# Kernel tuning notes

Hardware: AMD Instinct MI355X
Metric: run time of the kernel (lower is better)

## Reference

```python
import jax, jax.numpy as jnp
import numpy as np

N = 50000
E = 800000
IN_DIM = 256
HID = 64
HEADS = 4
OUT = 64
NEG_SLOPE = 0.2


def _gat_layer(x, src, dst, W, a_src, a_dst, b, heads, out_ch, concat):
    n = x.shape[0]
    h = (x @ W).reshape(n, heads, out_ch)                      # [N,H,C]
    al_src = jnp.sum(h * a_src, axis=-1)                       # [N,H]
    al_dst = jnp.sum(h * a_dst, axis=-1)                       # [N,H]
    e = jax.nn.leaky_relu(al_src[src] + al_dst[dst], NEG_SLOPE)  # [E,H]
    # segment softmax over destination nodes
    m = jax.ops.segment_max(e, dst, num_segments=n)
    m = jnp.where(jnp.isfinite(m), m, 0.0)
    ex = jnp.exp(e - m[dst])
    denom = jax.ops.segment_sum(ex, dst, num_segments=n)
    alpha = ex / (denom[dst] + 1e-16)                          # [E,H]
    msg = h[src] * alpha[:, :, None]                           # [E,H,C]
    out = jax.ops.segment_sum(msg, dst, num_segments=n)        # [N,H,C]
    out = out.reshape(n, heads * out_ch) if concat else out.mean(axis=1)
    return out + b


def setup_inputs() -> dict:
    key = jax.random.key(0)
    ks = jax.random.split(key, 16)
    x = jax.random.normal(ks[0], (N, IN_DIM), dtype=jnp.float32)
    edge_index = jax.random.randint(ks[1], (2, E), 0, N, dtype=jnp.int64)

    def glorot(k, shape):
        fan = shape[0] + shape[-1]
        s = jnp.sqrt(6.0 / fan).astype(jnp.float32)
        return jax.random.uniform(k, shape, jnp.float32, -s, s)

    # layer 1: IN_DIM -> HID x HEADS (concat)
    W1 = glorot(ks[2], (IN_DIM, HEADS * HID))
    a_src1 = glorot(ks[3], (HEADS, HID))
    a_dst1 = glorot(ks[4], (HEADS, HID))
    b1 = jnp.zeros((HEADS * HID,), jnp.float32)
    # layer 2: HID*HEADS -> HID x HEADS (concat)
    W2 = glorot(ks[5], (HEADS * HID, HEADS * HID))
    a_src2 = glorot(ks[6], (HEADS, HID))
    a_dst2 = glorot(ks[7], (HEADS, HID))
    b2 = jnp.zeros((HEADS * HID,), jnp.float32)
    # layer 3: HID*HEADS -> OUT, 1 head, concat=False
    W3 = glorot(ks[8], (HEADS * HID, OUT))
    a_src3 = glorot(ks[9], (1, OUT))
    a_dst3 = glorot(ks[10], (1, OUT))
    b3 = jnp.zeros((OUT,), jnp.float32)

    return {"x": x, "edge_index": edge_index,
            "W1": W1, "a_src1": a_src1, "a_dst1": a_dst1, "b1": b1,
            "W2": W2, "a_src2": a_src2, "a_dst2": a_dst2, "b2": b2,
            "W3": W3, "a_src3": a_src3, "a_dst3": a_dst3, "b3": b3}


def reference(x, edge_index, W1, a_src1, a_dst1, b1, W2, a_src2, a_dst2, b2, W3, a_src3, a_dst3, b3):
    src, dst = edge_index[0], edge_index[1]
    h = _gat_layer(x, src, dst, W1, a_src1, a_dst1, b1, HEADS, HID, True)
    h = jax.nn.elu(h)
    h = _gat_layer(h, src, dst, W2, a_src2, a_dst2, b2, HEADS, HID, True)
    h = jax.nn.elu(h)
    h = _gat_layer(h, src, dst, W3, a_src3, a_dst3, b3, 1, OUT, False)
    h = jax.nn.elu(h)
    return h
```

## Files before the change

### kernel.cpp

```cpp
#include <hip/hip_runtime.h>
#include <hip/hip_bf16.h>
#include <math.h>

#define IN_DIM 256
#define HID 64
#define HEADS 4
#define HC (HEADS * HID)
#define OUTC 64
#define NEG_SLOPE 0.2f

typedef unsigned int uint;
typedef unsigned short ushortt;
typedef __attribute__((ext_vector_type(8))) short short8v;
typedef __attribute__((ext_vector_type(4))) float floatx4;

union U8 { uint u[4]; short8v v; };

__device__ __forceinline__ float lrelu(float x) {
    return x >= 0.f ? x : NEG_SLOPE * x;
}
__device__ __forceinline__ float elu1(float x) {
    return x > 0.f ? x : expm1f(x);
}
__device__ __forceinline__ ushortt f2bf(float f) {
    uint x = __float_as_uint(f);
    uint r = (x + 0x7fffu + ((x >> 16) & 1u)) >> 16;
    return (ushortt)r;
}
__device__ __forceinline__ float bf2f(ushortt u) {
    return __uint_as_float(((uint)u) << 16);
}

#define CVTPAIR(fx, fy, ho, qo)                                                 \
    asm("v_cvt_pk_bf16_f32 %0, %1, %2" : "=v"(ho) : "v"(fx), "v"(fy));          \
    {                                                                           \
        float _r0 = (fx) - __uint_as_float((ho) << 16);                         \
        float _r1 = (fy) - __uint_as_float((ho) & 0xffff0000u);                 \
        asm("v_cvt_pk_bf16_f32 %0, %1, %2" : "=v"(qo) : "v"(_r0), "v"(_r1));    \
    }

__device__ __forceinline__ void wsplit_body(const float* __restrict__ W,
                                            ushortt* __restrict__ Wt, int N,
                                            int b, int tid) {
    int idx = b * 256 + tid;
    int j = idx & 7;
    int col = (idx >> 3) % N;
    int kb = (idx >> 3) / N;
    float wv = W[(size_t)(kb * 8 + j) * N + col];
    ushortt hi = f2bf(wv);
    ushortt lo = f2bf(wv - bf2f(hi));
    size_t o = ((size_t)kb * N + col) * 16 + j;
    Wt[o] = hi;
    Wt[o + 8] = lo;
}

__global__ __launch_bounds__(256) void count_prep(
        const float* __restrict__ W1, const float* __restrict__ W2,
        const float* __restrict__ W3,
        ushortt* __restrict__ Wt1, ushortt* __restrict__ Wt2,
        ushortt* __restrict__ Wt3,
        const int* __restrict__ dst, int* __restrict__ counts, int E) {
    int b = blockIdx.x, tid = threadIdx.x;
    if (b < 256) { wsplit_body(W1, Wt1, 256, b, tid); return; }
    if (b < 512) { wsplit_body(W2, Wt2, 256, b - 256, tid); return; }
    if (b < 576) { wsplit_body(W3, Wt3, 64, b - 512, tid); return; }
    int e = (b - 576) * 256 + tid;
    if (e < E) atomicAdd(&counts[dst[e]], 1);
}

#define SCAN_B 1024
__global__ void scan_block(const int* __restrict__ counts, int* __restrict__ ptr,
                           int* __restrict__ bsums, int n) {
    __shared__ int sm[SCAN_B];
    int b = blockIdx.x, t = threadIdx.x;
    int i = b * SCAN_B + t;
    int v = (i < n) ? counts[i] : 0;
    sm[t] = v;
    __syncthreads();
    for (int off = 1; off < SCAN_B; off <<= 1) {
        int add = (t >= off) ? sm[t - off] : 0;
        __syncthreads();
        sm[t] += add;
        __syncthreads();
    }
    if (i < n) ptr[i + 1] = sm[t];
    if (t == SCAN_B - 1) bsums[b] = sm[t];
}

__global__ void scan_add(int* __restrict__ ptr, const int* __restrict__ bsums,
                         int* __restrict__ work, int n) {
    __shared__ int pre;
    int seg = blockIdx.x >> 2;
    if (threadIdx.x == 0) {
        int s = 0;
        for (int b = 0; b < seg; b++) s += bsums[b];
        pre = s;
    }
    __syncthreads();
    int i = blockIdx.x * 256 + threadIdx.x;
    if (i == 0) { ptr[0] = 0; work[0] = 0; }
    if (i < n) {
        int v = ptr[i + 1] + pre;
        ptr[i + 1] = v;
        if (i + 1 < n) work[i + 1] = v;
    }
}

__global__ void scatter_edges(const int* __restrict__ src, const int* __restrict__ dst,
                              int* __restrict__ work, int* __restrict__ ssrc, int E) {
    int e = blockIdx.x * blockDim.x + threadIdx.x;
    if (e < E) {
        int p = atomicAdd(&work[dst[e]], 1);
        ssrc[p] = src[e] * 64;
    }
}

template<bool F32A>
__global__ __launch_bounds__(256, 3) void gemm_mfma(
        const ushortt* __restrict__ Ai, const float* __restrict__ Af,
        const ushortt* __restrict__ Wt,
        ushortt* __restrict__ Chi, int M,
        const float* __restrict__ a_src, const float* __restrict__ a_dst,
        float* __restrict__ alS, float* __restrict__ alD) {
    constexpr int N = 256;
    int t = threadIdx.x;
    int wid = t >> 6, l = t & 63, l15 = l & 15, chunk = l >> 4;
    int wr = wid >> 1, wc = wid & 1;
    int row0 = blockIdx.x * 64;
    int colw = wc * 128;

    floatx4 acc[2][8];
    floatx4 zero = {0.f, 0.f, 0.f, 0.f};
#pragma unroll
    for (int mt = 0; mt < 2; mt++)
#pragma unroll
        for (int nt = 0; nt < 8; nt++) acc[mt][nt] = zero;

    size_t arow[2];
#pragma unroll
    for (int mt = 0; mt < 2; mt++) {
        int r = row0 + wr * 32 + mt * 16 + l15;
        int rc = r < M ? r : M - 1;
        arow[mt] = F32A ? (size_t)rc * 256 : (size_t)rc * 512;
    }

    for (int ks = 0; ks < 8; ks++) {
        int kb = ks * 4 + chunk;
        short8v ah[2], aq[2];
        if constexpr (F32A) {
#pragma unroll
            for (int mt = 0; mt < 2; mt++) {
                const float* ap = Af + arow[mt] + kb * 8;
                float4 a0 = ((const float4*)ap)[0];
                float4 a1 = ((const float4*)ap)[1];
                U8 h, q;
                CVTPAIR(a0.x, a0.y, h.u[0], q.u[0]);
                CVTPAIR(a0.z, a0.w, h.u[1], q.u[1]);
                CVTPAIR(a1.x, a1.y, h.u[2], q.u[2]);
                CVTPAIR(a1.z, a1.w, h.u[3], q.u[3]);
                ah[mt] = h.v; aq[mt] = q.v;
            }
        } else {
#pragma unroll
            for (int mt = 0; mt < 2; mt++) {
                const ushortt* ap = Ai + arow[mt] + kb * 16;
                ah[mt] = *(const short8v*)ap;
                aq[mt] = *(const short8v*)(ap + 8);
            }
        }
        const ushortt* bbase = Wt + ((size_t)kb * N + colw + l15) * 16;
#pragma unroll
        for (int half = 0; half < 2; half++) {
            short8v bh[4], bq[4];
#pragma unroll
            for (int nt = 0; nt < 4; nt++) {
                const ushortt* bp = bbase + (size_t)(half * 4 + nt) * 256;
                bh[nt] = *(const short8v*)bp;
                bq[nt] = *(const short8v*)(bp + 8);
            }
#pragma unroll
            for (int mt = 0; mt < 2; mt++)
#pragma unroll
                for (int nt = 0; nt < 4; nt++) {
                    int c = half * 4 + nt;
                    acc[mt][c] = __builtin_amdgcn_mfma_f32_16x16x32_bf16(aq[mt], bh[nt], acc[mt][c], 0, 0, 0);
                    acc[mt][c] = __builtin_amdgcn_mfma_f32_16x16x32_bf16(ah[mt], bq[nt], acc[mt][c], 0, 0, 0);
                    acc[mt][c] = __builtin_amdgcn_mfma_f32_16x16x32_bf16(ah[mt], bh[nt], acc[mt][c], 0, 0, 0);
                }
        }
    }

#pragma unroll
    for (int mt = 0; mt < 2; mt++)
#pragma unroll
        for (int j = 0; j < 4; j++) {
            int r = row0 + wr * 32 + mt * 16 + chunk * 4 + j;
            if (r < M) {
#pragma unroll
                for (int nt = 0; nt < 8; nt++)
                    Chi[(size_t)r * N + colw + nt * 16 + l15] = f2bf(acc[mt][nt][j]);
            }
        }

    {
        float aSv[8], aDv[8];
#pragma unroll
        for (int nt = 0; nt < 8; nt++) {
            aSv[nt] = a_src[colw + nt * 16 + l15];
            aDv[nt] = a_dst[colw + nt * 16 + l15];
        }
#pragma unroll
        for (int mt = 0; mt < 2; mt++)
#pragma unroll
            for (int j = 0; j < 4; j++) {
                float s0 = 0.f, d0 = 0.f, s1 = 0.f, d1 = 0.f;
#pragma unroll
                for (int nt = 0; nt < 4; nt++) {
                    s0 += acc[mt][nt][j] * aSv[nt];
                    d0 += acc[mt][nt][j] * aDv[nt];
                    s1 += acc[mt][nt + 4][j] * aSv[nt + 4];
                    d1 += acc[mt][nt + 4][j] * aDv[nt + 4];
                }
#pragma unroll
                for (int off = 1; off < 16; off <<= 1) {
                    s0 += __shfl_xor(s0, off);
                    d0 += __shfl_xor(d0, off);
                    s1 += __shfl_xor(s1, off);
                    d1 += __shfl_xor(d1, off);
                }
                int r = row0 + wr * 32 + mt * 16 + chunk * 4 + j;
                if (l15 == 0 && r < M) {
                    alS[(size_t)r * 4 + wc * 2 + 0] = s0;
                    alS[(size_t)r * 4 + wc * 2 + 1] = s1;
                    alD[(size_t)r * 4 + wc * 2 + 0] = d0;
                    alD[(size_t)r * 4 + wc * 2 + 1] = d1;
                }
            }
    }
}

__global__ __launch_bounds__(256) void gemm_n64(
        const ushortt* __restrict__ Ai, const ushortt* __restrict__ Wt,
        ushortt* __restrict__ Chi, int M,
        const float* __restrict__ a_src, const float* __restrict__ a_dst,
        float* __restrict__ alS, float* __restrict__ alD) {
    constexpr int N = 64;
    int t = threadIdx.x;
    int wid = t >> 6, l = t & 63, l15 = l & 15, chunk = l >> 4;
    int row0 = blockIdx.x * 64;
    int rw = row0 + wid * 16 + l15;
    size_t arow = (size_t)(rw < M ? rw : M - 1) * 512;

    floatx4 acc[4];
    floatx4 zero = {0.f, 0.f, 0.f, 0.f};
#pragma unroll
    for (int nt = 0; nt < 4; nt++) acc[nt] = zero;

    for (int ks = 0; ks < 8; ks++) {
        int kb = ks * 4 + chunk;
        short8v bh[4], bq[4];
#pragma unroll
        for (int nt = 0; nt < 4; nt++) {
            const ushortt* bp = Wt + ((size_t)kb * N + nt * 16 + l15) * 16;
            bh[nt] = *(const short8v*)bp;
            bq[nt] = *(const short8v*)(bp + 8);
        }
        const ushortt* ap = Ai + arow + kb * 16;
        short8v ah = *(const short8v*)ap;
        short8v aq = *(const short8v*)(ap + 8);
#pragma unroll
        for (int nt = 0; nt < 4; nt++) {
            acc[nt] = __builtin_amdgcn_mfma_f32_16x16x32_bf16(aq, bh[nt], acc[nt], 0, 0, 0);
            acc[nt] = __builtin_amdgcn_mfma_f32_16x16x32_bf16(ah, bq[nt], acc[nt], 0, 0, 0);
            acc[nt] = __builtin_amdgcn_mfma_f32_16x16x32_bf16(ah, bh[nt], acc[nt], 0, 0, 0);
        }
    }

    float aSv[4], aDv[4];
#pragma unroll
    for (int nt = 0; nt < 4; nt++) {
        aSv[nt] = a_src[nt * 16 + l15];
        aDv[nt] = a_dst[nt * 16 + l15];
    }
#pragma unroll
    for (int j = 0; j < 4; j++) {
        int r = row0 + wid * 16 + chunk * 4 + j;
        if (r < M) {
#pragma unroll
            for (int nt = 0; nt < 4; nt++)
                Chi[(size_t)r * N + nt * 16 + l15] = f2bf(acc[nt][j]);
        }
        float s = 0.f, d = 0.f;
#pragma unroll
        for (int nt = 0; nt < 4; nt++) {
            s += acc[nt][j] * aSv[nt];
            d += acc[nt][j] * aDv[nt];
        }
#pragma unroll
        for (int off = 1; off < 16; off <<= 1) {
            s += __shfl_xor(s, off);
            d += __shfl_xor(d, off);
        }
        if (l15 == 0 && r < M) {
            alS[r] = s;
            alD[r] = d;
        }
    }
}

__global__ __launch_bounds__(256) void gather4f(
        const float* __restrict__ alS, const float* __restrict__ alD,
        const ushortt* __restrict__ h,
        const int* __restrict__ ptr, const int* __restrict__ ssrc,
        const float* __restrict__ bias, ushortt* __restrict__ outAi, int n) {
    int w = threadIdx.x >> 6, lane = threadIdx.x & 63;
    int node = blockIdx.x * 4 + w;
    if (node >= n) return;
    int p0 = ptr[node], p1 = ptr[node + 1];
    int head = lane >> 4;
    float adh = alD[node * 4 + head];
    const ushort4* h4 = (const ushort4*)h;
    float4 acc0 = make_float4(0.f, 0.f, 0.f, 0.f);
    float4 acc1 = make_float4(0.f, 0.f, 0.f, 0.f);
    float sum = 0.f;

    int i = p0;
#pragma unroll 1
    for (; i + 8 <= p1; i += 8) {
        int o0 = ssrc[i+0], o1 = ssrc[i+1], o2 = ssrc[i+2], o3 = ssrc[i+3];
        int o4 = ssrc[i+4], o5 = ssrc[i+5], o6 = ssrc[i+6], o7 = ssrc[i+7];
        float w0 = __expf(lrelu(alS[(o0 >> 4) + head] + adh));
        float w1 = __expf(lrelu(alS[(o1 >> 4) + head] + adh));
        float w2 = __expf(lrelu(alS[(o2 >> 4) + head] + adh));
        float w3 = __expf(lrelu(alS[(o3 >> 4) + head] + adh));
        float w4 = __expf(lrelu(alS[(o4 >> 4) + head] + adh));
        float w5 = __expf(lrelu(alS[(o5 >> 4) + head] + adh));
        float w6 = __expf(lrelu(alS[(o6 >> 4) + head] + adh));
        float w7 = __expf(lrelu(alS[(o7 >> 4) + head] + adh));
        ushort4 u0 = h4[o0 + lane];
        ushort4 u1 = h4[o1 + lane];
        ushort4 u2 = h4[o2 + lane];
        ushort4 u3 = h4[o3 + lane];
        ushort4 u4 = h4[o4 + lane];
        ushort4 u5 = h4[o5 + lane];
        ushort4 u6 = h4[o6 + lane];
        ushort4 u7 = h4[o7 + lane];
        sum += w0 + w1 + w2 + w3 + w4 + w5 + w6 + w7;
        acc0.x += bf2f(u0.x)*w0; acc0.y += bf2f(u0.y)*w0; acc0.z += bf2f(u0.z)*w0; acc0.w += bf2f(u0.w)*w0;
        acc1.x += bf2f(u1.x)*w1; acc1.y += bf2f(u1.y)*w1; acc1.z += bf2f(u1.z)*w1; acc1.w += bf2f(u1.w)*w1;
        acc0.x += bf2f(u2.x)*w2; acc0.y += bf2f(u2.y)*w2; acc0.z += bf2f(u2.z)*w2; acc0.w += bf2f(u2.w)*w2;
        acc1.x += bf2f(u3.x)*w3; acc1.y += bf2f(u3.y)*w3; acc1.z += bf2f(u3.z)*w3; acc1.w += bf2f(u3.w)*w3;
        acc0.x += bf2f(u4.x)*w4; acc0.y += bf2f(u4.y)*w4; acc0.z += bf2f(u4.z)*w4; acc0.w += bf2f(u4.w)*w4;
        acc1.x += bf2f(u5.x)*w5; acc1.y += bf2f(u5.y)*w5; acc1.z += bf2f(u5.z)*w5; acc1.w += bf2f(u5.w)*w5;
        acc0.x += bf2f(u6.x)*w6; acc0.y += bf2f(u6.y)*w6; acc0.z += bf2f(u6.z)*w6; acc0.w += bf2f(u6.w)*w6;
        acc1.x += bf2f(u7.x)*w7; acc1.y += bf2f(u7.y)*w7; acc1.z += bf2f(u7.z)*w7; acc1.w += bf2f(u7.w)*w7;
    }
#pragma unroll 1
    for (; i < p1; ++i) {
        int o0 = ssrc[i];
        float w0 = __expf(lrelu(alS[(o0 >> 4) + head] + adh));
        ushort4 u0 = h4[o0 + lane];
        sum += w0;
        acc0.x += bf2f(u0.x)*w0; acc0.y += bf2f(u0.y)*w0; acc0.z += bf2f(u0.z)*w0; acc0.w += bf2f(u0.w)*w0;
    }
    float invh = 1.f / (sum + 1e-16f);
    acc0.x = (acc0.x + acc1.x) * invh;
    acc0.y = (acc0.y + acc1.y) * invh;
    acc0.z = (acc0.z + acc1.z) * invh;
    acc0.w = (acc0.w + acc1.w) * invh;

    float4 b = ((const float4*)bias)[lane];
    float4 o;
    o.x = elu1(acc0.x + b.x);
    o.y = elu1(acc0.y + b.y);
    o.z = elu1(acc0.z + b.z);
    o.w = elu1(acc0.w + b.w);
    ushort4 oh, oq;
    oh.x = f2bf(o.x); oq.x = f2bf(o.x - bf2f(oh.x));
    oh.y = f2bf(o.y); oq.y = f2bf(o.y - bf2f(oh.y));
    oh.z = f2bf(o.z); oq.z = f2bf(o.z - bf2f(oh.z));
    oh.w = f2bf(o.w); oq.w = f2bf(o.w - bf2f(oh.w));
    size_t base = (size_t)node * 512 + (lane >> 1) * 16 + (lane & 1) * 4;
    *(ushort4*)&outAi[base] = oh;
    *(ushort4*)&outAi[base + 8] = oq;
}

__global__ __launch_bounds__(256) void gather1f(
        const float* __restrict__ alS, const float* __restrict__ alD,
        const ushortt* __restrict__ h,
        const int* __restrict__ ptr, const int* __restrict__ ssrc,
        const float* __restrict__ bias, float* __restrict__ out, int n) {
    int w = threadIdx.x >> 6, lane = threadIdx.x & 63;
    int node = blockIdx.x * 4 + w;
    if (node >= n) return;
    int p0 = ptr[node], p1 = ptr[node + 1];
    float ad = alD[node];
    int eslot = lane >> 4, cg = lane & 15;
    const ushort4* h4 = (const ushort4*)h;
    float4 acc = make_float4(0.f, 0.f, 0.f, 0.f);
    float sum = 0.f;

#pragma unroll 1
    for (int i = p0 + eslot; i < p1; i += 4) {
        int o = ssrc[i];
        float wv = __expf(lrelu(alS[o >> 6] + ad));
        ushort4 u = h4[(o >> 2) + cg];
        sum += wv;
        acc.x += bf2f(u.x) * wv;
        acc.y += bf2f(u.y) * wv;
        acc.z += bf2f(u.z) * wv;
        acc.w += bf2f(u.w) * wv;
    }
#pragma unroll
    for (int off = 16; off < 64; off <<= 1) {
        acc.x += __shfl_xor(acc.x, off);
        acc.y += __shfl_xor(acc.y, off);
        acc.z += __shfl_xor(acc.z, off);
        acc.w += __shfl_xor(acc.w, off);
        sum   += __shfl_xor(sum, off);
    }
    if (eslot == 0) {
        float inv = 1.f / (sum + 1e-16f);
        float4 b = ((const float4*)bias)[cg];
        float4 o;
        o.x = elu1(acc.x * inv + b.x);
        o.y = elu1(acc.y * inv + b.y);
        o.z = elu1(acc.z * inv + b.z);
        o.w = elu1(acc.w * inv + b.w);
        ((float4*)out)[node * 16 + cg] = o;
    }
}

extern "C" void kernel_launch(void* const* d_in, const int* in_sizes, int n_in,
                              void* d_out, int out_size, void* d_ws, size_t ws_size,
                              hipStream_t stream) {
    const float* x      = (const float*)d_in[0];
    const int*   eidx   = (const int*)d_in[1];
    const float* W1     = (const float*)d_in[2];
    const float* a_src1 = (const float*)d_in[3];
    const float* a_dst1 = (const float*)d_in[4];
    const float* b1     = (const float*)d_in[5];
    const float* W2     = (const float*)d_in[6];
    const float* a_src2 = (const float*)d_in[7];
    const float* a_dst2 = (const float*)d_in[8];
    const float* b2     = (const float*)d_in[9];
    const float* W3     = (const float*)d_in[10];
    const float* a_src3 = (const float*)d_in[11];
    const float* a_dst3 = (const float*)d_in[12];
    const float* b3     = (const float*)d_in[13];

    const int n = in_sizes[0] / IN_DIM;
    const int E = in_sizes[1] / 2;
    const int* srcp = eidx;
    const int* dstp = eidx + E;

    size_t off = 0;
    auto alloc = [&](size_t bytes) {
        void* p = (char*)d_ws + off;
        off += (bytes + 255) & ~(size_t)255;
        return p;
    };
    int*     ptr    = (int*)alloc((size_t)(n + 1) * 4);
    int*     work   = (int*)alloc((size_t)n * 4);
    int*     bsums  = (int*)alloc(256 * 4);
    int*     ssrc   = (int*)alloc((size_t)E * 4);
    ushortt* Ai0    = (ushortt*)alloc((size_t)n * 512 * 2);
    ushortt* Ai1    = (ushortt*)alloc((size_t)n * 512 * 2);
    ushortt* hbf    = (ushortt*)alloc((size_t)n * HC * 2);
    float*   alS    = (float*)alloc((size_t)n * HEADS * 4);
    float*   alD    = (float*)alloc((size_t)n * HEADS * 4);
    ushortt* Wt1    = (ushortt*)alloc((size_t)256 * HC * 2 * 2);
    ushortt* Wt2    = (ushortt*)alloc((size_t)256 * HC * 2 * 2);
    ushortt* Wt3    = (ushortt*)alloc((size_t)256 * OUTC * 2 * 2);
    (void)ws_size;

    hipMemsetAsync(work, 0, (size_t)n * 4, stream);
    int cblocks = 576 + (E + 255) / 256;
    count_prep<<<cblocks, 256, 0, stream>>>(W1, W2, W3, Wt1, Wt2, Wt3,
                                            dstp, work, E);
    int nb = (n + SCAN_B - 1) / SCAN_B;
    scan_block<<<nb, SCAN_B, 0, stream>>>(work, ptr, bsums, n);
    scan_add<<<(n + 255) / 256, 256, 0, stream>>>(ptr, bsums, work, n);
    scatter_edges<<<(E + 255) / 256, 256, 0, stream>>>(srcp, dstp, work, ssrc, E);

    int gblocks = (n + 63) / 64;
    int node4 = (n + 3) / 4;

    gemm_mfma<true><<<gblocks, 256, 0, stream>>>(
        nullptr, x, Wt1, hbf, n, a_src1, a_dst1, alS, alD);
    gather4f<<<node4, 256, 0, stream>>>(alS, alD, hbf, ptr, ssrc, b1, Ai1, n);

    gemm_mfma<false><<<gblocks, 256, 0, stream>>>(
        Ai1, nullptr, Wt2, hbf, n, a_src2, a_dst2, alS, alD);
    gather4f<<<node4, 256, 0, stream>>>(alS, alD, hbf, ptr, ssrc, b2, Ai0, n);

    gemm_n64<<<gblocks, 256, 0, stream>>>(
        Ai0, Wt3, hbf, n, a_src3, a_dst3, alS, alD);
    gather1f<<<node4, 256, 0, stream>>>(alS, alD, hbf, ptr, ssrc, b3,
                                        (float*)d_out, n);
}
```

Baseline: 386.1 us.

## Fuse CSR block scan into first GEMM launch and dedupe attention weights in gather

The standalone block-scan kernel is removed and its work is done by extra trailing blocks of the first layer's GEMM launch, each scanning 1024 counts with 256 threads holding four values apiece. This saves a launch and lets the scan run alongside the GEMM. In gather4f, each lane now computes one edge's attention weight, and the eight weights are broadcast with shuffles instead of every lane doing eight redundant alS loads and exps. The gather block size also drops from 256 to 128 threads (two nodes per block), giving finer scheduling granularity at the cost of more blocks.

```diff
diff --git a/kernel.cpp b/kernel.cpp
--- a/kernel.cpp
+++ b/kernel.cpp
@@ -68,25 +68,6 @@
     if (e < E) atomicAdd(&counts[dst[e]], 1);
 }
 
-#define SCAN_B 1024
-__global__ void scan_block(const int* __restrict__ counts, int* __restrict__ ptr,
-                           int* __restrict__ bsums, int n) {
-    __shared__ int sm[SCAN_B];
-    int b = blockIdx.x, t = threadIdx.x;
-    int i = b * SCAN_B + t;
-    int v = (i < n) ? counts[i] : 0;
-    sm[t] = v;
-    __syncthreads();
-    for (int off = 1; off < SCAN_B; off <<= 1) {
-        int add = (t >= off) ? sm[t - off] : 0;
-        __syncthreads();
-        sm[t] += add;
-        __syncthreads();
-    }
-    if (i < n) ptr[i + 1] = sm[t];
-    if (t == SCAN_B - 1) bsums[b] = sm[t];
-}
-
 __global__ void scan_add(int* __restrict__ ptr, const int* __restrict__ bsums,
                          int* __restrict__ work, int n) {
     __shared__ int pre;
@@ -121,8 +102,40 @@
         const ushortt* __restrict__ Wt,
         ushortt* __restrict__ Chi, int M,
         const float* __restrict__ a_src, const float* __restrict__ a_dst,
-        float* __restrict__ alS, float* __restrict__ alD) {
+        float* __restrict__ alS, float* __restrict__ alD,
+        const int* __restrict__ counts, int* __restrict__ ptrOut,
+        int* __restrict__ bsums, int nScan, int gemmBlocks) {
     constexpr int N = 256;
+    if constexpr (F32A) {
+        if ((int)blockIdx.x >= gemmBlocks) {
+            __shared__ int sm[256];
+            int sb = blockIdx.x - gemmBlocks;
+            int t = threadIdx.x;
+            int i = sb * 1024 + t * 4;
+            int v0 = 0, v1 = 0, v2 = 0, v3 = 0;
+            if (i + 0 < nScan) v0 = counts[i + 0];
+            if (i + 1 < nScan) v1 = counts[i + 1];
+            if (i + 2 < nScan) v2 = counts[i + 2];
+            if (i + 3 < nScan) v3 = counts[i + 3];
+            int s1 = v0 + v1, s2 = s1 + v2, s3 = s2 + v3;
+            sm[t] = s3;
+            __syncthreads();
+            for (int off = 1; off < 256; off <<= 1) {
+                int add = (t >= off) ? sm[t - off] : 0;
+                __syncthreads();
+                sm[t] += add;
+                __syncthreads();
+            }
+            int pre = (t > 0) ? sm[t - 1] : 0;
+            if (i + 0 < nScan) ptrOut[i + 1] = pre + v0;
+            if (i + 1 < nScan) ptrOut[i + 2] = pre + s1;
+            if (i + 2 < nScan) ptrOut[i + 3] = pre + s2;
+            if (i + 3 < nScan) ptrOut[i + 4] = pre + s3;
+            if (t == 255) bsums[sb] = sm[255];
+            return;
+        }
+    }
+
     int t = threadIdx.x;
     int wid = t >> 6, l = t & 63, l15 = l & 15, chunk = l >> 4;
     int wr = wid >> 1, wc = wid & 1;
@@ -308,16 +321,17 @@
     }
 }
 
-__global__ __launch_bounds__(256) void gather4f(
+__global__ __launch_bounds__(128) void gather4f(
         const float* __restrict__ alS, const float* __restrict__ alD,
         const ushortt* __restrict__ h,
         const int* __restrict__ ptr, const int* __restrict__ ssrc,
         const float* __restrict__ bias, ushortt* __restrict__ outAi, int n) {
     int w = threadIdx.x >> 6, lane = threadIdx.x & 63;
-    int node = blockIdx.x * 4 + w;
+    int node = blockIdx.x * 2 + w;
     if (node >= n) return;
     int p0 = ptr[node], p1 = ptr[node + 1];
     int head = lane >> 4;
+    int gbase = lane & 48;
     float adh = alD[node * 4 + head];
     const ushort4* h4 = (const ushort4*)h;
     float4 acc0 = make_float4(0.f, 0.f, 0.f, 0.f);
@@ -329,14 +343,16 @@
     for (; i + 8 <= p1; i += 8) {
         int o0 = ssrc[i+0], o1 = ssrc[i+1], o2 = ssrc[i+2], o3 = ssrc[i+3];
         int o4 = ssrc[i+4], o5 = ssrc[i+5], o6 = ssrc[i+6], o7 = ssrc[i+7];
-        float w0 = __expf(lrelu(alS[(o0 >> 4) + head] + adh));
-        float w1 = __expf(lrelu(alS[(o1 >> 4) + head] + adh));
-        float w2 = __expf(lrelu(alS[(o2 >> 4) + head] + adh));
-        float w3 = __expf(lrelu(alS[(o3 >> 4) + head] + adh));
-        float w4 = __expf(lrelu(alS[(o4 >> 4) + head] + adh));
-        float w5 = __expf(lrelu(alS[(o5 >> 4) + head] + adh));
-        float w6 = __expf(lrelu(alS[(o6 >> 4) + head] + adh));
-        float w7 = __expf(lrelu(alS[(o7 >> 4) + head] + adh));
+        int oj = ssrc[i + (lane & 7)];
+        float wme = __expf(lrelu(alS[(oj >> 4) + head] + adh));
+        float w0 = __shfl(wme, gbase + 0);
+        float w1 = __shfl(wme, gbase + 1);
+        float w2 = __shfl(wme, gbase + 2);
+        float w3 = __shfl(wme, gbase + 3);
+        float w4 = __shfl(wme, gbase + 4);
+        float w5 = __shfl(wme, gbase + 5);
+        float w6 = __shfl(wme, gbase + 6);
+        float w7 = __shfl(wme, gbase + 7);
         ushort4 u0 = h4[o0 + lane];
         ushort4 u1 = h4[o1 + lane];
         ushort4 u2 = h4[o2 + lane];
@@ -478,21 +494,24 @@
     int cblocks = 576 + (E + 255) / 256;
     count_prep<<<cblocks, 256, 0, stream>>>(W1, W2, W3, Wt1, Wt2, Wt3,
                                             dstp, work, E);
-    int nb = (n + SCAN_B - 1) / SCAN_B;
-    scan_block<<<nb, SCAN_B, 0, stream>>>(work, ptr, bsums, n);
+
+    int gblocks = (n + 63) / 64;
+    int nb = (n + 1023) / 1024;
+    int node2 = (n + 1) / 2;
+    int node4 = (n + 3) / 4;
+
+    gemm_mfma<true><<<gblocks + nb, 256, 0, stream>>>(
+        nullptr, x, Wt1, hbf, n, a_src1, a_dst1, alS, alD,
+        work, ptr, bsums, n, gblocks);
     scan_add<<<(n + 255) / 256, 256, 0, stream>>>(ptr, bsums, work, n);
     scatter_edges<<<(E + 255) / 256, 256, 0, stream>>>(srcp, dstp, work, ssrc, E);
 
-    int gblocks = (n + 63) / 64;
-    int node4 = (n + 3) / 4;
-
-    gemm_mfma<true><<<gblocks, 256, 0, stream>>>(
-        nullptr, x, Wt1, hbf, n, a_src1, a_dst1, alS, alD);
-    gather4f<<<node4, 256, 0, stream>>>(alS, alD, hbf, ptr, ssrc, b1, Ai1, n);
+    gather4f<<<node2, 128, 0, stream>>>(alS, alD, hbf, ptr, ssrc, b1, Ai1, n);
 
     gemm_mfma<false><<<gblocks, 256, 0, stream>>>(
-        Ai1, nullptr, Wt2, hbf, n, a_src2, a_dst2, alS, alD);
-    gather4f<<<node4, 256, 0, stream>>>(alS, alD, hbf, ptr, ssrc, b2, Ai0, n);
+        Ai1, nullptr, Wt2, hbf, n, a_src2, a_dst2, alS, alD,
+        nullptr, nullptr, nullptr, 0, gblocks);
+    gather4f<<<node2, 128, 0, stream>>>(alS, alD, hbf, ptr, ssrc, b2, Ai0, n);
 
     gemm_n64<<<gblocks, 256, 0, stream>>>(
         Ai0, Wt3, hbf, n, a_src3, a_dst3, alS, alD);
```

New measurement: 370.0 us. 1.04x faster.
